# Optimization experiments

Hardware: AMD Instinct MI355X
Metric: run time of the kernel (lower is better)

The kernel has to match this reference:

```python
import jax, jax.numpy as jnp
import numpy as np

B, LQ, LK = 8, 2048, 2048
D_IN, D_KQ, D_OUT = 512, 512, 512


def setup_inputs() -> dict:
    key = jax.random.key(0)
    ks = jax.random.split(key, 8)
    s = 0.02
    return {
        "x_1": jax.random.normal(ks[0], (B, LQ, D_IN), jnp.float32),
        "x_2": jax.random.normal(ks[1], (B, LK, D_IN), jnp.float32),
        "Wq": jax.random.normal(ks[2], (D_IN, D_KQ), jnp.float32) * s,
        "bq": jax.random.normal(ks[3], (D_KQ,), jnp.float32) * s,
        "Wk": jax.random.normal(ks[4], (D_IN, D_KQ), jnp.float32) * s,
        "bk": jax.random.normal(ks[5], (D_KQ,), jnp.float32) * s,
        "Wv": jax.random.normal(ks[6], (D_IN, D_OUT), jnp.float32) * s,
        "bv": jax.random.normal(ks[7], (D_OUT,), jnp.float32) * s,
    }


def reference(x_1, x_2, Wq, bq, Wk, bk, Wv, bv):
    q = x_1 @ Wq + bq                      # [B, LQ, D_KQ]
    k = x_2 @ Wk + bk                      # [B, LK, D_KQ]
    v = x_2 @ Wv + bv                      # [B, LK, D_OUT]
    scores = jnp.einsum('bqd,bkd->bqk', q, k) / jnp.sqrt(jnp.float32(D_KQ))
    attn = jax.nn.softmax(scores, axis=-1)  # [B, LQ, LK]
    return jnp.einsum('bqk,bkd->bqd', attn, v)
```

## Files before the change

kernel.cpp:

```cpp
#include <hip/hip_runtime.h>
#include <hip/hip_bf16.h>
#include <stdint.h>

typedef __attribute__((ext_vector_type(8))) short bf16x8;
typedef __attribute__((ext_vector_type(4))) float f32x4;

#define MFMA16(a, b, c) __builtin_amdgcn_mfma_f32_16x16x32_bf16((a), (b), (c), 0, 0, 0)

__device__ __forceinline__ unsigned short f2bf(float f) {
    union { float f; uint32_t u; } c; c.f = f;
    uint32_t u = c.u + 0x7fffu + ((c.u >> 16) & 1u);
    return (unsigned short)(u >> 16);
}

__device__ __forceinline__ void gll16(const void* g, void* l) {
    __builtin_amdgcn_global_load_lds((const __attribute__((address_space(1))) void*)g,
                                     (__attribute__((address_space(3))) void*)l, 16, 0, 0);
}

__global__ void wtrans_kernel(const float* __restrict__ Wq, const float* __restrict__ Wk,
                              const float* __restrict__ Wv,
                              unsigned short* __restrict__ WqT, unsigned short* __restrict__ WkT,
                              unsigned short* __restrict__ WvT) {
    __shared__ float tile[32][33];
    const int z = blockIdx.z;
    const float* W = (z == 0) ? Wq : ((z == 1) ? Wk : Wv);
    unsigned short* WT = (z == 0) ? WqT : ((z == 1) ? WkT : WvT);
    const int k0 = blockIdx.x * 32, n0 = blockIdx.y * 32;
    const int tx = threadIdx.x, ty = threadIdx.y;
#pragma unroll
    for (int i = ty; i < 32; i += 8)
        tile[i][tx] = W[(size_t)(k0 + i) * 512 + n0 + tx];
    __syncthreads();
#pragma unroll
    for (int i = ty; i < 32; i += 8)
        WT[(size_t)(n0 + i) * 512 + k0 + tx] = f2bf(tile[tx][i]);
}

__global__ __launch_bounds__(512) void proj_kernel(
        const float* __restrict__ x1, const float* __restrict__ x2,
        const unsigned short* __restrict__ WqT, const unsigned short* __restrict__ WkT,
        const unsigned short* __restrict__ WvT,
        const float* __restrict__ bq, const float* __restrict__ bk, const float* __restrict__ bv,
        unsigned short* __restrict__ Qb, unsigned short* __restrict__ Kb,
        unsigned short* __restrict__ Vtb) {
    extern __shared__ __align__(16) char psm[];
    const int z = blockIdx.z;
    const float* X = (z == 0) ? x1 : x2;
    const unsigned short* WT = (z == 0) ? WqT : ((z == 1) ? WkT : WvT);
    const float* bias = (z == 0) ? bq : ((z == 1) ? bk : bv);

    const int tid = threadIdx.x, w = tid >> 6, lane = tid & 63;
    const int l15 = lane & 15, g = lane >> 4;
    const int mb = blockIdx.x * 64, nb = blockIdx.y * 256;

    const int xm = tid >> 3, xk8 = (tid & 7) * 8;
    const int awcol = ((tid & 7) * 16) ^ (((tid >> 3) & 7) << 4);
    const int wcol = ((lane & 7) * 16) ^ (((lane >> 3) & 7) << 4);
    const int l7x16 = (l15 & 7) << 4;

    const float* Xrow = X + (size_t)(mb + xm) * 512 + xk8;
    const char* Wbase = (const char*)WT + (size_t)(nb + (lane >> 3)) * 1024 + wcol;

    f32x4 acc[4][2] = {};
    float4 xr0[2], xr1[2];

    xr0[0] = *(const float4*)(Xrow);
    xr0[1] = *(const float4*)(Xrow + 4);
#pragma unroll
    for (int c = 0; c < 4; ++c)
        gll16(Wbase + (size_t)(w * 32 + c * 8) * 1024,
              psm + 16384 + (w * 32 + c * 8) * 128);

#define PROJ_STEP(KT, XC, XN, AOFF, BOFF, BNOFF)                               \
    {                                                                          \
        if ((KT) < 7) {                                                        \
            const float* xs = Xrow + ((KT) + 1) * 64;                          \
            XN[0] = *(const float4*)xs;                                        \
            XN[1] = *(const float4*)(xs + 4);                                  \
            _Pragma("unroll")                                                  \
            for (int c = 0; c < 4; ++c)                                        \
                gll16(Wbase + ((KT) + 1) * 128 + (size_t)(w * 32 + c * 8) * 1024, \
                      psm + (BNOFF) + (w * 32 + c * 8) * 128);                 \
            asm volatile("s_waitcnt vmcnt(6)" ::: "memory");                   \
        } else {                                                               \
            asm volatile("s_waitcnt vmcnt(0)" ::: "memory");                   \
        }                                                                      \
        {                                                                      \
            uint32_t p0 = f2bf(XC[0].x) | ((uint32_t)f2bf(XC[0].y) << 16);     \
            uint32_t p1 = f2bf(XC[0].z) | ((uint32_t)f2bf(XC[0].w) << 16);     \
            uint32_t p2 = f2bf(XC[1].x) | ((uint32_t)f2bf(XC[1].y) << 16);     \
            uint32_t p3 = f2bf(XC[1].z) | ((uint32_t)f2bf(XC[1].w) << 16);     \
            int4 av; av.x = p0; av.y = p1; av.z = p2; av.w = p3;               \
            *(int4*)(psm + (AOFF) + xm * 128 + awcol) = av;                    \
        }                                                                      \
        asm volatile("s_waitcnt lgkmcnt(0)" ::: "memory");                     \
        __builtin_amdgcn_sched_barrier(0);                                     \
        __builtin_amdgcn_s_barrier();                                          \
        __builtin_amdgcn_sched_barrier(0);                                     \
        _Pragma("unroll")                                                      \
        for (int ks = 0; ks < 2; ++ks) {                                       \
            bf16x8 af[4], bfr[2];                                              \
            _Pragma("unroll")                                                  \
            for (int rb = 0; rb < 4; ++rb)                                     \
                af[rb] = *(const bf16x8*)(psm + (AOFF) + (rb * 16 + l15) * 128 \
                                          + ((ks * 64 + g * 16) ^ l7x16));     \
            _Pragma("unroll")                                                  \
            for (int cb = 0; cb < 2; ++cb)                                     \
                bfr[cb] = *(const bf16x8*)(psm + (BOFF)                        \
                           + (w * 32 + cb * 16 + l15) * 128                    \
                           + ((ks * 64 + g * 16) ^ l7x16));                    \
            _Pragma("unroll")                                                  \
            for (int rb = 0; rb < 4; ++rb)                                     \
                _Pragma("unroll")                                              \
                for (int cb = 0; cb < 2; ++cb)                                 \
                    acc[rb][cb] = MFMA16(af[rb], bfr[cb], acc[rb][cb]);        \
        }                                                                      \
        __builtin_amdgcn_sched_barrier(0);                                     \
        __builtin_amdgcn_s_barrier();                                          \
        __builtin_amdgcn_sched_barrier(0);                                     \
    }

    PROJ_STEP(0, xr0, xr1, 0,    16384, 49152)
    PROJ_STEP(1, xr1, xr0, 8192, 49152, 16384)
    PROJ_STEP(2, xr0, xr1, 0,    16384, 49152)
    PROJ_STEP(3, xr1, xr0, 8192, 49152, 16384)
    PROJ_STEP(4, xr0, xr1, 0,    16384, 49152)
    PROJ_STEP(5, xr1, xr0, 8192, 49152, 16384)
    PROJ_STEP(6, xr0, xr1, 0,    16384, 49152)
    PROJ_STEP(7, xr1, xr0, 8192, 49152, 16384)
#undef PROJ_STEP

    if (z < 2) {
        unsigned short* O = (z == 0) ? Qb : Kb;
#pragma unroll
        for (int cb = 0; cb < 2; ++cb) {
            const int n = nb + w * 32 + cb * 16 + l15;
            const float bn = bias[n];
#pragma unroll
            for (int rb = 0; rb < 4; ++rb)
#pragma unroll
                for (int r = 0; r < 4; ++r)
                    O[(size_t)(mb + rb * 16 + g * 4 + r) * 512 + n] =
                        f2bf(acc[rb][cb][r] + bn);
        }
    } else {
        char* Tr = psm;
#pragma unroll
        for (int cb = 0; cb < 2; ++cb) {
            const int nl = w * 32 + cb * 16 + l15;
            const float bn = bias[nb + nl];
#pragma unroll
            for (int rb = 0; rb < 4; ++rb)
#pragma unroll
                for (int r = 0; r < 4; ++r) {
                    const int m2 = (rb * 16 + g * 4 + r) * 2;
                    *(unsigned short*)(Tr + nl * 128 + (m2 ^ l7x16)) =
                        f2bf(acc[rb][cb][r] + bn);
                }
        }
        asm volatile("s_waitcnt lgkmcnt(0)" ::: "memory");
        __builtin_amdgcn_sched_barrier(0);
        __builtin_amdgcn_s_barrier();
        __builtin_amdgcn_sched_barrier(0);
        const int bidx = mb >> 11, kv0 = mb & 2047;
#pragma unroll
        for (int it = 0; it < 4; ++it) {
            const int idx = it * 512 + tid;
            const int n2 = idx >> 3, t8 = idx & 7;
            int4 v = *(const int4*)(Tr + n2 * 128 + ((t8 * 16) ^ ((n2 & 7) << 4)));
            *(int4*)(Vtb + ((size_t)bidx * 512 + nb + n2) * 2048 + kv0 + t8 * 8) = v;
        }
    }
}

#define ATTN_SCALE 0.04419417382415922f
#define ATTN_LDS_BYTES 139776

__global__ __attribute__((amdgpu_waves_per_eu(2, 2))) __launch_bounds__(512)
void attn_kernel(const unsigned short* __restrict__ Q,
                 const unsigned short* __restrict__ K,
                 const unsigned short* __restrict__ Vt,
                 float* __restrict__ out) {
    extern __shared__ __align__(16) char smem[];
    char* Kb = smem;
    char* Vb = smem + 65536;
    char* Ps = smem + 131072;
    float* lred = (float*)(smem + 139264);

    const int tid = threadIdx.x, w = tid >> 6, lane = tid & 63;
    const int l15 = lane & 15, g = lane >> 4;
    const int b = blockIdx.x, qb0 = blockIdx.y * 64;
    const int rb = w >> 1, h = w & 1;
    const int l7x16 = (l15 & 7) << 4;

    const char* Kg = (const char*)K + (size_t)b * 2048 * 1024;
    const char* Vg = (const char*)Vt + (size_t)b * 512 * 4096;
    const int vcol = ((lane & 7) * 16) ^ (((lane >> 3) & 7) << 4);
    const int vrow = lane >> 3;

#pragma unroll
    for (int c = 0; c < 8; ++c) {
        const int r = w * 8 + c;
        gll16(Kg + (size_t)r * 1024 + ((lane * 16) ^ (c << 4)), Kb + r * 1024);
    }
    bf16x8 qreg[16];
    {
        const char* qbase = (const char*)Q +
            ((size_t)b * 2048 + qb0 + rb * 16 + l15) * 1024 + g * 16;
#pragma unroll
        for (int dk = 0; dk < 16; ++dk)
            qreg[dk] = *(const bf16x8*)(qbase + dk * 64);
    }

    f32x4 acc[4][4] = {};
    float lsum[4] = {0.f, 0.f, 0.f, 0.f};

    for (int kt = 0; kt < 32; ++kt) {
        asm volatile("s_waitcnt vmcnt(0)" ::: "memory");
        asm volatile("s_waitcnt lgkmcnt(0)" ::: "memory");
        __builtin_amdgcn_sched_barrier(0);
        __builtin_amdgcn_s_barrier();
        __builtin_amdgcn_sched_barrier(0);

        {
            const char* vg = Vg + (size_t)kt * 128;
#pragma unroll
            for (int c = 0; c < 8; ++c) {
                const int r0 = w * 64 + c * 8;
                gll16(vg + (size_t)(r0 + vrow) * 4096 + vcol, Vb + r0 * 128);
            }
        }

        const char* kbr0 = Kb + (size_t)(h * 32 + l15) * 1024;
        const char* kbr1 = kbr0 + 16 * 1024;
        f32x4 s0 = {}, s1 = {};
#pragma unroll
        for (int dk = 0; dk < 16; ++dk) {
            const int off = (dk * 64 + g * 16) ^ l7x16;
            bf16x8 kf0 = *(const bf16x8*)(kbr0 + off);
            bf16x8 kf1 = *(const bf16x8*)(kbr1 + off);
            s0 = MFMA16(qreg[dk], kf0, s0);
            s1 = MFMA16(qreg[dk], kf1, s1);
        }

        asm volatile("s_waitcnt lgkmcnt(0)" ::: "memory");
        __builtin_amdgcn_sched_barrier(0);
        __builtin_amdgcn_s_barrier();
        __builtin_amdgcn_sched_barrier(0);

        if (kt < 31) {
            const char* kg = Kg + (size_t)(kt + 1) * 65536;
#pragma unroll
            for (int c = 0; c < 8; ++c) {
                const int r = w * 8 + c;
                gll16(kg + (size_t)r * 1024 + ((lane * 16) ^ (c << 4)), Kb + r * 1024);
            }
        }

#pragma unroll
        for (int r = 0; r < 4; ++r) {
            const float p0 = __expf(s0[r] * ATTN_SCALE);
            const float p1 = __expf(s1[r] * ATTN_SCALE);
            lsum[r] += p0 + p1;
            const int q = rb * 16 + g * 4 + r;
            const int xk = (q & 7) << 4;
            const int c0 = (h * 32 + l15) * 2;
            *(unsigned short*)(Ps + q * 128 + (c0 ^ xk)) = f2bf(p0);
            *(unsigned short*)(Ps + q * 128 + ((c0 + 32) ^ xk)) = f2bf(p1);
        }

        if (kt < 31) {
            asm volatile("s_waitcnt vmcnt(8)" ::: "memory");
        } else {
            asm volatile("s_waitcnt vmcnt(0)" ::: "memory");
        }
        asm volatile("s_waitcnt lgkmcnt(0)" ::: "memory");
        __builtin_amdgcn_sched_barrier(0);
        __builtin_amdgcn_s_barrier();
        __builtin_amdgcn_sched_barrier(0);

#pragma unroll
        for (int ks2 = 0; ks2 < 2; ++ks2) {
            const int off2 = (ks2 * 64 + g * 16) ^ l7x16;
            bf16x8 pa[4];
#pragma unroll
            for (int qb = 0; qb < 4; ++qb)
                pa[qb] = *(const bf16x8*)(Ps + (size_t)(qb * 16 + l15) * 128 + off2);
#pragma unroll
            for (int dvb = 0; dvb < 4; ++dvb) {
                bf16x8 vf = *(const bf16x8*)(Vb + (size_t)(w * 64 + dvb * 16 + l15) * 128 + off2);
#pragma unroll
                for (int qb = 0; qb < 4; ++qb)
                    acc[qb][dvb] = MFMA16(pa[qb], vf, acc[qb][dvb]);
            }
        }
    }

    asm volatile("s_waitcnt vmcnt(0)" ::: "memory");

#pragma unroll
    for (int r = 0; r < 4; ++r) {
        float v = lsum[r];
        v += __shfl_xor(v, 1); v += __shfl_xor(v, 2);
        v += __shfl_xor(v, 4); v += __shfl_xor(v, 8);
        lsum[r] = v;
    }
    if (l15 == 0) {
#pragma unroll
        for (int r = 0; r < 4; ++r)
            lred[h * 64 + rb * 16 + g * 4 + r] = lsum[r];
    }
    __syncthreads();

    float* outb = out + ((size_t)b * 2048 + qb0) * 512 + w * 64;
#pragma unroll
    for (int qb = 0; qb < 4; ++qb)
#pragma unroll
        for (int r = 0; r < 4; ++r) {
            const int q = qb * 16 + g * 4 + r;
            const float linv = 1.0f / (lred[q] + lred[64 + q]);
#pragma unroll
            for (int dvb = 0; dvb < 4; ++dvb)
                outb[(size_t)q * 512 + dvb * 16 + l15] = acc[qb][dvb][r] * linv;
        }
}

extern "C" void kernel_launch(void* const* d_in, const int* in_sizes, int n_in,
                              void* d_out, int out_size, void* d_ws, size_t ws_size,
                              hipStream_t stream) {
    const float* x1 = (const float*)d_in[0];
    const float* x2 = (const float*)d_in[1];
    const float* Wq = (const float*)d_in[2];
    const float* bq = (const float*)d_in[3];
    const float* Wk = (const float*)d_in[4];
    const float* bk = (const float*)d_in[5];
    const float* Wv = (const float*)d_in[6];
    const float* bv = (const float*)d_in[7];
    float* out = (float*)d_out;

    char* ws = (char*)d_ws;
    unsigned short* Qb  = (unsigned short*)(ws);
    unsigned short* Kb  = (unsigned short*)(ws + 16777216);
    unsigned short* Vtb = (unsigned short*)(ws + 33554432);
    unsigned short* WqT = (unsigned short*)(ws + 50331648);
    unsigned short* WkT = (unsigned short*)(ws + 50331648 + 524288);
    unsigned short* WvT = (unsigned short*)(ws + 50331648 + 1048576);

    wtrans_kernel<<<dim3(16, 16, 3), dim3(32, 8), 0, stream>>>(Wq, Wk, Wv, WqT, WkT, WvT);

    hipFuncSetAttribute((const void*)proj_kernel,
                        hipFuncAttributeMaxDynamicSharedMemorySize, 81920);
    proj_kernel<<<dim3(256, 2, 3), 512, 81920, stream>>>(x1, x2, WqT, WkT, WvT,
                                                         bq, bk, bv, Qb, Kb, Vtb);

    hipFuncSetAttribute((const void*)attn_kernel,
                        hipFuncAttributeMaxDynamicSharedMemorySize, ATTN_LDS_BYTES);
    attn_kernel<<<dim3(8, 32), 512, ATTN_LDS_BYTES, stream>>>(Qb, Kb, Vtb, out);
}
```

Measured before the change: 243.5 us.

## Load V fragments into registers, double-buffer K in LDS, deepen X prefetch

In the attention kernel, V tiles no longer go through LDS. Each lane loads its own V fragments from global memory into registers, and the next tile's fragments are prefetched after the PV MFMAs. K now uses the freed LDS space as a double buffer, so the next K tile loads at the start of each iteration and one barrier per iteration is removed. The projection kernel prefetches X two steps ahead with triple-buffered registers and adjusted vmcnt waits, at the cost of more VGPR pressure and uncoalesced-ish direct V global loads.

```diff
diff --git a/kernel.cpp b/kernel.cpp
--- a/kernel.cpp
+++ b/kernel.cpp
@@ -63,29 +63,31 @@
     const char* Wbase = (const char*)WT + (size_t)(nb + (lane >> 3)) * 1024 + wcol;
 
     f32x4 acc[4][2] = {};
-    float4 xr0[2], xr1[2];
-
-    xr0[0] = *(const float4*)(Xrow);
-    xr0[1] = *(const float4*)(Xrow + 4);
+    float4 x0[2], x1r[2], x2r[2];
+
+    x0[0] = *(const float4*)(Xrow);
+    x0[1] = *(const float4*)(Xrow + 4);
+    x1r[0] = *(const float4*)(Xrow + 64);
+    x1r[1] = *(const float4*)(Xrow + 68);
 #pragma unroll
     for (int c = 0; c < 4; ++c)
         gll16(Wbase + (size_t)(w * 32 + c * 8) * 1024,
               psm + 16384 + (w * 32 + c * 8) * 128);
 
-#define PROJ_STEP(KT, XC, XN, AOFF, BOFF, BNOFF)                               \
+#define PROJ_STEP(KT, XC, XN2, AOFF, BOFF, BNOFF, WAITN, DO_W, DO_X)           \
     {                                                                          \
-        if ((KT) < 7) {                                                        \
-            const float* xs = Xrow + ((KT) + 1) * 64;                          \
-            XN[0] = *(const float4*)xs;                                        \
-            XN[1] = *(const float4*)(xs + 4);                                  \
+        if (DO_W) {                                                            \
             _Pragma("unroll")                                                  \
             for (int c = 0; c < 4; ++c)                                        \
                 gll16(Wbase + ((KT) + 1) * 128 + (size_t)(w * 32 + c * 8) * 1024, \
                       psm + (BNOFF) + (w * 32 + c * 8) * 128);                 \
-            asm volatile("s_waitcnt vmcnt(6)" ::: "memory");                   \
-        } else {                                                               \
-            asm volatile("s_waitcnt vmcnt(0)" ::: "memory");                   \
         }                                                                      \
+        if (DO_X) {                                                            \
+            const float* xs = Xrow + ((KT) + 2) * 64;                          \
+            XN2[0] = *(const float4*)xs;                                       \
+            XN2[1] = *(const float4*)(xs + 4);                                 \
+        }                                                                      \
+        asm volatile("s_waitcnt vmcnt(" #WAITN ")" ::: "memory");              \
         {                                                                      \
             uint32_t p0 = f2bf(XC[0].x) | ((uint32_t)f2bf(XC[0].y) << 16);     \
             uint32_t p1 = f2bf(XC[0].z) | ((uint32_t)f2bf(XC[0].w) << 16);     \
@@ -121,14 +123,14 @@
         __builtin_amdgcn_sched_barrier(0);                                     \
     }
 
-    PROJ_STEP(0, xr0, xr1, 0,    16384, 49152)
-    PROJ_STEP(1, xr1, xr0, 8192, 49152, 16384)
-    PROJ_STEP(2, xr0, xr1, 0,    16384, 49152)
-    PROJ_STEP(3, xr1, xr0, 8192, 49152, 16384)
-    PROJ_STEP(4, xr0, xr1, 0,    16384, 49152)
-    PROJ_STEP(5, xr1, xr0, 8192, 49152, 16384)
-    PROJ_STEP(6, xr0, xr1, 0,    16384, 49152)
-    PROJ_STEP(7, xr1, xr0, 8192, 49152, 16384)
+    PROJ_STEP(0, x0,  x2r, 0,    16384, 49152, 6, 1, 1)
+    PROJ_STEP(1, x1r, x0,  8192, 49152, 16384, 8, 1, 1)
+    PROJ_STEP(2, x2r, x1r, 0,    16384, 49152, 8, 1, 1)
+    PROJ_STEP(3, x0,  x2r, 8192, 49152, 16384, 8, 1, 1)
+    PROJ_STEP(4, x1r, x0,  0,    16384, 49152, 8, 1, 1)
+    PROJ_STEP(5, x2r, x1r, 8192, 49152, 16384, 8, 1, 1)
+    PROJ_STEP(6, x0,  x2r, 0,    16384, 49152, 6, 1, 0)
+    PROJ_STEP(7, x1r, x0,  8192, 49152, 16384, 0, 0, 0)
 #undef PROJ_STEP
 
     if (z < 2) {
@@ -183,8 +185,6 @@
                  const unsigned short* __restrict__ Vt,
                  float* __restrict__ out) {
     extern __shared__ __align__(16) char smem[];
-    char* Kb = smem;
-    char* Vb = smem + 65536;
     char* Ps = smem + 131072;
     float* lred = (float*)(smem + 139264);
 
@@ -195,14 +195,12 @@
     const int l7x16 = (l15 & 7) << 4;
 
     const char* Kg = (const char*)K + (size_t)b * 2048 * 1024;
-    const char* Vg = (const char*)Vt + (size_t)b * 512 * 4096;
-    const int vcol = ((lane & 7) * 16) ^ (((lane >> 3) & 7) << 4);
-    const int vrow = lane >> 3;
+    const char* Vg = (const char*)Vt + (size_t)b * 2097152;
 
 #pragma unroll
     for (int c = 0; c < 8; ++c) {
         const int r = w * 8 + c;
-        gll16(Kg + (size_t)r * 1024 + ((lane * 16) ^ (c << 4)), Kb + r * 1024);
+        gll16(Kg + (size_t)r * 1024 + ((lane * 16) ^ (c << 4)), smem + r * 1024);
     }
     bf16x8 qreg[16];
     {
@@ -212,27 +210,37 @@
         for (int dk = 0; dk < 16; ++dk)
             qreg[dk] = *(const bf16x8*)(qbase + dk * 64);
     }
+    bf16x8 vreg[2][4];
+    const char* Vlane = Vg + (size_t)(w * 64 + l15) * 4096 + g * 16;
+#pragma unroll
+    for (int ks2 = 0; ks2 < 2; ++ks2)
+#pragma unroll
+        for (int dvb = 0; dvb < 4; ++dvb)
+            vreg[ks2][dvb] = *(const bf16x8*)(Vlane + dvb * 65536 + ks2 * 64);
 
     f32x4 acc[4][4] = {};
     float lsum[4] = {0.f, 0.f, 0.f, 0.f};
 
     for (int kt = 0; kt < 32; ++kt) {
-        asm volatile("s_waitcnt vmcnt(0)" ::: "memory");
+        asm volatile("s_waitcnt vmcnt(8)" ::: "memory");
         asm volatile("s_waitcnt lgkmcnt(0)" ::: "memory");
         __builtin_amdgcn_sched_barrier(0);
         __builtin_amdgcn_s_barrier();
         __builtin_amdgcn_sched_barrier(0);
 
-        {
-            const char* vg = Vg + (size_t)kt * 128;
+        const char* kbuf = smem + (size_t)(kt & 1) * 65536;
+
+        if (kt < 31) {
+            char* kb = smem + (size_t)((kt + 1) & 1) * 65536;
+            const char* kg = Kg + (size_t)(kt + 1) * 65536;
 #pragma unroll
             for (int c = 0; c < 8; ++c) {
-                const int r0 = w * 64 + c * 8;
-                gll16(vg + (size_t)(r0 + vrow) * 4096 + vcol, Vb + r0 * 128);
+                const int r = w * 8 + c;
+                gll16(kg + (size_t)r * 1024 + ((lane * 16) ^ (c << 4)), kb + r * 1024);
             }
         }
 
-        const char* kbr0 = Kb + (size_t)(h * 32 + l15) * 1024;
+        const char* kbr0 = kbuf + (size_t)(h * 32 + l15) * 1024;
         const char* kbr1 = kbr0 + 16 * 1024;
         f32x4 s0 = {}, s1 = {};
 #pragma unroll
@@ -242,20 +250,6 @@
             bf16x8 kf1 = *(const bf16x8*)(kbr1 + off);
             s0 = MFMA16(qreg[dk], kf0, s0);
             s1 = MFMA16(qreg[dk], kf1, s1);
-        }
-
-        asm volatile("s_waitcnt lgkmcnt(0)" ::: "memory");
-        __builtin_amdgcn_sched_barrier(0);
-        __builtin_amdgcn_s_barrier();
-        __builtin_amdgcn_sched_barrier(0);
-
-        if (kt < 31) {
-            const char* kg = Kg + (size_t)(kt + 1) * 65536;
-#pragma unroll
-            for (int c = 0; c < 8; ++c) {
-                const int r = w * 8 + c;
-                gll16(kg + (size_t)r * 1024 + ((lane * 16) ^ (c << 4)), Kb + r * 1024);
-            }
         }
 
 #pragma unroll
@@ -288,16 +282,21 @@
             for (int qb = 0; qb < 4; ++qb)
                 pa[qb] = *(const bf16x8*)(Ps + (size_t)(qb * 16 + l15) * 128 + off2);
 #pragma unroll
-            for (int dvb = 0; dvb < 4; ++dvb) {
-                bf16x8 vf = *(const bf16x8*)(Vb + (size_t)(w * 64 + dvb * 16 + l15) * 128 + off2);
+            for (int dvb = 0; dvb < 4; ++dvb)
 #pragma unroll
                 for (int qb = 0; qb < 4; ++qb)
-                    acc[qb][dvb] = MFMA16(pa[qb], vf, acc[qb][dvb]);
-            }
-        }
-    }
-
-    asm volatile("s_waitcnt vmcnt(0)" ::: "memory");
+                    acc[qb][dvb] = MFMA16(pa[qb], vreg[ks2][dvb], acc[qb][dvb]);
+        }
+
+        if (kt < 31) {
+            const char* vn = Vlane + (size_t)(kt + 1) * 128;
+#pragma unroll
+            for (int ks2 = 0; ks2 < 2; ++ks2)
+#pragma unroll
+                for (int dvb = 0; dvb < 4; ++dvb)
+                    vreg[ks2][dvb] = *(const bf16x8*)(vn + dvb * 65536 + ks2 * 64);
+        }
+    }
 
 #pragma unroll
     for (int r = 0; r < 4; ++r) {
```

New measurement: 278.8 us. +14.5%, slower.
